# Optimization experiments

Hardware: AMD Instinct MI355X
Metric: run time of the kernel (lower is better)

The kernel has to match this reference:

```python
import jax, jax.numpy as jnp
import numpy as np

N = 100000
D = 128
E = 1600000
NUM_STEPS = 8
LAM0 = 1.0
LAM1 = 1.0
ALPHA = 1.0 / (1.0 + 0.0 + LAM0 + LAM1)  # args.alp == 0 path


def setup_inputs() -> dict:
    key = jax.random.key(0)
    ks = jax.random.split(key, 12)
    X = jax.random.normal(ks[0], (N, D), dtype=jnp.float32)
    # H init: normal(0, 1/in_features) + I  (notresidual=False branch)
    H1 = jax.random.normal(ks[1], (D, D), dtype=jnp.float32) * (1.0 / D) + jnp.eye(D, dtype=jnp.float32)
    H2 = jax.random.normal(ks[2], (D, D), dtype=jnp.float32) * (1.0 / D) + jnp.eye(D, dtype=jnp.float32)
    w_beta = jax.random.uniform(ks[3], (E,), dtype=jnp.float32)
    w_gamma = jax.random.uniform(ks[4], (E,), dtype=jnp.float32)
    d_beta = jax.random.uniform(ks[5], (N,), dtype=jnp.float32)
    d_gamma = jax.random.uniform(ks[6], (N,), dtype=jnp.float32)
    src_beta = jax.random.randint(ks[7], (E,), 0, N, dtype=jnp.int32)
    dst_beta = jax.random.randint(ks[8], (E,), 0, N, dtype=jnp.int32)
    src_gamma = jax.random.randint(ks[9], (E,), 0, N, dtype=jnp.int32)
    dst_gamma = jax.random.randint(ks[10], (E,), 0, N, dtype=jnp.int32)
    return {"X": X, "H1": H1, "H2": H2, "w_beta": w_beta, "w_gamma": w_gamma,
            "d_beta": d_beta, "d_gamma": d_gamma,
            "src_beta": src_beta, "dst_beta": dst_beta,
            "src_gamma": src_gamma, "dst_gamma": dst_gamma}


def _spmm(w, src, dst, Y):
    # (sparse A) @ Y with A[dst, src] = w
    return jax.ops.segment_sum(w[:, None] * Y[src], dst, num_segments=N)


def reference(X, H1, H2, w_beta, w_gamma, d_beta, d_gamma,
              src_beta, dst_beta, src_gamma, dst_gamma):
    # Q_tild = lam0*D_beta + lam1*D_gamma + I  (diagonal)
    q = LAM0 * d_beta + LAM1 * d_gamma + 1.0  # [N]
    S1 = H1 + H1.T
    P1 = H1 @ H1.T
    S2 = H2 + H2.T
    P2 = H2 @ H2.T
    Y0 = X
    Y = X
    for _ in range(NUM_STEPS):
        AbY = _spmm(w_beta, src_beta, dst_beta, Y)    # A_beta @ Y
        AgY = _spmm(w_gamma, src_gamma, dst_gamma, Y)  # A_gamma @ Y
        term_beta = AbY @ S1 - d_beta[:, None] * (Y @ P1)
        # L_gamma @ Y = D_gamma@Y - A_gamma@Y
        term_gamma = (d_gamma[:, None] * Y - AgY
                      + AgY @ S2 - d_gamma[:, None] * (Y @ P2))
        Y_hat = LAM0 * term_beta + Y0 + LAM1 * term_gamma
        Y = (1.0 - ALPHA) * Y + ALPHA * (Y_hat / q[:, None])
    return Y
```

## Files before the change

### kernel.cpp

```cpp
#include <hip/hip_runtime.h>
#include <cstdint>
#include <cstddef>

#define DD 128
#define ATS 68
#define WTS 130


__global__ void count2_k(const int* __restrict__ dstb, const int* __restrict__ dstg,
                         int* __restrict__ degb, int* __restrict__ degg, int E, int gE) {
    int b = blockIdx.x;
    const int* dst = (b < gE) ? dstb : dstg;
    int* deg = (b < gE) ? degb : degg;
    int i = ((b < gE) ? b : b - gE) * blockDim.x + threadIdx.x;
    if (i < E) atomicAdd(&deg[dst[i]], 1);
}

__global__ __launch_bounds__(1024) void scan2_k(const int* __restrict__ degb,
                                                const int* __restrict__ degg,
                                                int* __restrict__ rpb, int* __restrict__ rpg,
                                                int* __restrict__ curb, int* __restrict__ curg,
                                                int n) {
    const int* deg = (blockIdx.x == 0) ? degb : degg;
    int* rp = (blockIdx.x == 0) ? rpb : rpg;
    int* cur = (blockIdx.x == 0) ? curb : curg;
    __shared__ int sums[1024];
    int tid = threadIdx.x;
    int per = (n + 1023) >> 10;
    int start = tid * per;
    int end = min(start + per, n);
    int s = 0;
    for (int i = start; i < end; ++i) s += deg[i];
    sums[tid] = s;
    __syncthreads();
    for (int off = 1; off < 1024; off <<= 1) {
        int v = (tid >= off) ? sums[tid - off] : 0;
        __syncthreads();
        sums[tid] += v;
        __syncthreads();
    }
    int pre = (tid == 0) ? 0 : sums[tid - 1];
    for (int i = start; i < end; ++i) {
        rp[i] = pre;
        cur[i] = pre;
        pre += deg[i];
    }
    if (end == n) rp[n] = pre;
}

__global__ void fill2_k(const int* __restrict__ srcb, const int* __restrict__ dstb,
                        const float* __restrict__ wb,
                        const int* __restrict__ srcg, const int* __restrict__ dstg,
                        const float* __restrict__ wg,
                        int* __restrict__ curb, int* __restrict__ curg,
                        int2* __restrict__ eb, int2* __restrict__ eg, int E, int gE) {
    int b = blockIdx.x;
    bool isb = (b < gE);
    const int* src = isb ? srcb : srcg;
    const int* dst = isb ? dstb : dstg;
    const float* w = isb ? wb : wg;
    int* cur = isb ? curb : curg;
    int2* edges = isb ? eb : eg;
    int i = (isb ? b : b - gE) * blockDim.x + threadIdx.x;
    if (i < E) {
        int d = dst[i];
        int pos = atomicAdd(&cur[d], 1);
        edges[pos] = make_int2(src[i], __float_as_int(w[i]));
    }
}


__global__ __launch_bounds__(256) void prep_k(const float* __restrict__ H,
                                              float* __restrict__ P,
                                              float* __restrict__ S) {
    int idx = blockIdx.x * 256 + threadIdx.x;
    int i = idx >> 7, j = idx & 127;
    float acc = 0.f;
    for (int k = 0; k < DD; ++k) acc += H[i * DD + k] * H[j * DD + k];
    P[idx] = acc;
    S[idx] = H[i * DD + j] + H[j * DD + i];
}


__global__ __launch_bounds__(256, 8) void spmm2_k(
    const int* __restrict__ rpb, const int2* __restrict__ eb,
    const int* __restrict__ rpg, const int2* __restrict__ eg,
    const float* __restrict__ Y,
    float* __restrict__ outb, float* __restrict__ outg, int n)
{
    int node = blockIdx.x * 4 + (threadIdx.x >> 6);
    if (node >= n) return;
    int lane = threadIdx.x & 63;

    int jb = rpb[node], be = rpb[node + 1];
    int jg = rpg[node], ge = rpg[node + 1];
    float b0 = 0.f, b1 = 0.f, g0 = 0.f, g1 = 0.f;

    while (jb + 4 <= be && jg + 4 <= ge) {
        int2 x0 = eb[jb + 0], x1 = eb[jb + 1], x2 = eb[jb + 2], x3 = eb[jb + 3];
        int2 y0 = eg[jg + 0], y1 = eg[jg + 1], y2 = eg[jg + 2], y3 = eg[jg + 3];
        float2 fb0 = *((const float2*)(Y + (size_t)x0.x * DD) + lane);
        float2 fb1 = *((const float2*)(Y + (size_t)x1.x * DD) + lane);
        float2 fb2 = *((const float2*)(Y + (size_t)x2.x * DD) + lane);
        float2 fb3 = *((const float2*)(Y + (size_t)x3.x * DD) + lane);
        float2 fg0 = *((const float2*)(Y + (size_t)y0.x * DD) + lane);
        float2 fg1 = *((const float2*)(Y + (size_t)y1.x * DD) + lane);
        float2 fg2 = *((const float2*)(Y + (size_t)y2.x * DD) + lane);
        float2 fg3 = *((const float2*)(Y + (size_t)y3.x * DD) + lane);
        float wb0 = __int_as_float(x0.y), wb1 = __int_as_float(x1.y);
        float wb2 = __int_as_float(x2.y), wb3 = __int_as_float(x3.y);
        float wg0 = __int_as_float(y0.y), wg1 = __int_as_float(y1.y);
        float wg2 = __int_as_float(y2.y), wg3 = __int_as_float(y3.y);
        b0 += wb0 * fb0.x; b1 += wb0 * fb0.y;
        b0 += wb1 * fb1.x; b1 += wb1 * fb1.y;
        b0 += wb2 * fb2.x; b1 += wb2 * fb2.y;
        b0 += wb3 * fb3.x; b1 += wb3 * fb3.y;
        g0 += wg0 * fg0.x; g1 += wg0 * fg0.y;
        g0 += wg1 * fg1.x; g1 += wg1 * fg1.y;
        g0 += wg2 * fg2.x; g1 += wg2 * fg2.y;
        g0 += wg3 * fg3.x; g1 += wg3 * fg3.y;
        jb += 4; jg += 4;
    }
    while (jb + 4 <= be) {
        int2 x0 = eb[jb + 0], x1 = eb[jb + 1], x2 = eb[jb + 2], x3 = eb[jb + 3];
        float2 f0 = *((const float2*)(Y + (size_t)x0.x * DD) + lane);
        float2 f1 = *((const float2*)(Y + (size_t)x1.x * DD) + lane);
        float2 f2 = *((const float2*)(Y + (size_t)x2.x * DD) + lane);
        float2 f3 = *((const float2*)(Y + (size_t)x3.x * DD) + lane);
        float w0 = __int_as_float(x0.y), w1 = __int_as_float(x1.y);
        float w2 = __int_as_float(x2.y), w3 = __int_as_float(x3.y);
        b0 += w0 * f0.x; b1 += w0 * f0.y;
        b0 += w1 * f1.x; b1 += w1 * f1.y;
        b0 += w2 * f2.x; b1 += w2 * f2.y;
        b0 += w3 * f3.x; b1 += w3 * f3.y;
        jb += 4;
    }
    while (jg + 4 <= ge) {
        int2 y0 = eg[jg + 0], y1 = eg[jg + 1], y2 = eg[jg + 2], y3 = eg[jg + 3];
        float2 f0 = *((const float2*)(Y + (size_t)y0.x * DD) + lane);
        float2 f1 = *((const float2*)(Y + (size_t)y1.x * DD) + lane);
        float2 f2 = *((const float2*)(Y + (size_t)y2.x * DD) + lane);
        float2 f3 = *((const float2*)(Y + (size_t)y3.x * DD) + lane);
        float w0 = __int_as_float(y0.y), w1 = __int_as_float(y1.y);
        float w2 = __int_as_float(y2.y), w3 = __int_as_float(y3.y);
        g0 += w0 * f0.x; g1 += w0 * f0.y;
        g0 += w1 * f1.x; g1 += w1 * f1.y;
        g0 += w2 * f2.x; g1 += w2 * f2.y;
        g0 += w3 * f3.x; g1 += w3 * f3.y;
        jg += 4;
    }
    for (; jb < be; ++jb) {
        int2 e = eb[jb];
        float2 f = *((const float2*)(Y + (size_t)e.x * DD) + lane);
        float wv = __int_as_float(e.y);
        b0 += wv * f.x; b1 += wv * f.y;
    }
    for (; jg < ge; ++jg) {
        int2 e = eg[jg];
        float2 f = *((const float2*)(Y + (size_t)e.x * DD) + lane);
        float wv = __int_as_float(e.y);
        g0 += wv * f.x; g1 += wv * f.y;
    }
    *((float2*)(outb + (size_t)node * DD) + lane) = make_float2(b0, b1);
    *((float2*)(outg + (size_t)node * DD) + lane) = make_float2(g0, g1);
}


__global__ __launch_bounds__(1024, 8) void dense_vs_k(
    const float* __restrict__ Yc, const float* __restrict__ X,
    const float* __restrict__ AbY, const float* __restrict__ AgY,
    const float* __restrict__ db, const float* __restrict__ dg,
    const float* __restrict__ P1, const float* __restrict__ P2,
    const float* __restrict__ S1, const float* __restrict__ S2,
    float* __restrict__ Yn, int n)
{
    __shared__ float At[DD * ATS];

    const int tid  = threadIdx.x;
    const int lane = tid & 63;
    const int wid  = tid >> 6;
    const int cw   = wid << 3;
    const int c0   = __builtin_amdgcn_readfirstlane(cw);
    const int row0 = blockIdx.x * 64;
    const int rowc = min(row0 + lane, n - 1);

    auto stageT = [&](const float* __restrict__ G) {
        const float* gp = G + (size_t)rowc * DD + cw;
        float4 v0 = *reinterpret_cast<const float4*>(gp);
        float4 v1 = *reinterpret_cast<const float4*>(gp + 4);
        At[(cw + 0) * ATS + lane] = v0.x;
        At[(cw + 1) * ATS + lane] = v0.y;
        At[(cw + 2) * ATS + lane] = v0.z;
        At[(cw + 3) * ATS + lane] = v0.w;
        At[(cw + 4) * ATS + lane] = v1.x;
        At[(cw + 5) * ATS + lane] = v1.y;
        At[(cw + 6) * ATS + lane] = v1.z;
        At[(cw + 7) * ATS + lane] = v1.w;
    };

    const float dbv = db[rowc];
    const float dgv = dg[rowc];

    float acc[8];

    stageT(Yc);
    __syncthreads();

    {
        const float* xp = X + (size_t)rowc * DD + c0;
#pragma unroll
        for (int j = 0; j < 8; ++j)
            acc[j] = xp[j] + dgv * At[(c0 + j) * ATS + lane];
    }

    {
        const float* p1 = P1 + c0;
        const float* p2 = P2 + c0;
#pragma unroll 4
        for (int k = 0; k < DD; ++k) {
            float a = At[k * ATS + lane];
            float am1 = dbv * a;
            float am2 = dgv * a;
            const float* r1 = p1 + k * DD;
            const float* r2 = p2 + k * DD;
#pragma unroll
            for (int j = 0; j < 8; ++j)
                acc[j] -= am1 * r1[j] + am2 * r2[j];
        }
    }

    __syncthreads();
    stageT(AbY);
    __syncthreads();
    {
        const float* s1 = S1 + c0;
#pragma unroll 4
        for (int k = 0; k < DD; ++k) {
            float a = At[k * ATS + lane];
            const float* r = s1 + k * DD;
#pragma unroll
            for (int j = 0; j < 8; ++j)
                acc[j] += a * r[j];
        }
    }

    __syncthreads();
    stageT(AgY);
    __syncthreads();
    {
        const float* s2 = S2 + c0;
#pragma unroll 4
        for (int k = 0; k < DD; ++k) {
            float a = At[k * ATS + lane];
            const float* r = s2 + k * DD;
#pragma unroll
            for (int j = 0; j < 8; ++j)
                acc[j] += a * r[j];
        }
#pragma unroll
        for (int j = 0; j < 8; ++j)
            acc[j] -= At[(c0 + j) * ATS + lane];
    }

    {
        const float aq = (1.0f / 3.0f) / (dbv + dgv + 1.0f);
        const float* yp = Yc + (size_t)rowc * DD + c0;
#pragma unroll
        for (int j = 0; j < 8; ++j)
            acc[j] = (2.0f / 3.0f) * yp[j] + acc[j] * aq;
    }

    __syncthreads();
    {
        float* W = At;
#pragma unroll
        for (int j = 0; j < 8; ++j)
            W[lane * WTS + cw + j] = acc[j];
    }
    __syncthreads();
    {
        const float* W = At;
        int r2 = tid >> 4;
        int c2 = (tid & 15) << 3;
        int row2 = row0 + r2;
        if (row2 < n) {
            float ov[8];
#pragma unroll
            for (int j = 0; j < 8; ++j) ov[j] = W[r2 * WTS + c2 + j];
            float* op = Yn + (size_t)row2 * DD + c2;
            *reinterpret_cast<float4*>(op) = make_float4(ov[0], ov[1], ov[2], ov[3]);
            *reinterpret_cast<float4*>(op + 4) = make_float4(ov[4], ov[5], ov[6], ov[7]);
        }
    }
}


extern "C" void kernel_launch(void* const* d_in, const int* in_sizes, int n_in,
                              void* d_out, int out_size, void* d_ws, size_t ws_size,
                              hipStream_t stream) {
    const float* X   = (const float*)d_in[0];
    const float* H1  = (const float*)d_in[1];
    const float* H2  = (const float*)d_in[2];
    const float* wb  = (const float*)d_in[3];
    const float* wg  = (const float*)d_in[4];
    const float* db  = (const float*)d_in[5];
    const float* dg  = (const float*)d_in[6];
    const int* srcb  = (const int*)d_in[7];
    const int* dstb  = (const int*)d_in[8];
    const int* srcg  = (const int*)d_in[9];
    const int* dstg  = (const int*)d_in[10];
    const int N = in_sizes[5];
    const int E = in_sizes[3];
    float* Yout = (float*)d_out;

    char* p = (char*)d_ws;
    auto alloc = [&](size_t b) -> void* {
        void* r = (void*)p;
        p += (b + 255) & ~(size_t)255;
        return r;
    };
    float* P1 = (float*)alloc((size_t)DD * DD * 4);
    float* S1 = (float*)alloc((size_t)DD * DD * 4);
    float* P2 = (float*)alloc((size_t)DD * DD * 4);
    float* S2 = (float*)alloc((size_t)DD * DD * 4);
    int* degb = (int*)alloc((size_t)N * 4);
    int* degg = (int*)alloc((size_t)N * 4);
    int* rpb  = (int*)alloc((size_t)(N + 1) * 4);
    int* rpg  = (int*)alloc((size_t)(N + 1) * 4);
    int* curb = (int*)alloc((size_t)N * 4);
    int* curg = (int*)alloc((size_t)N * 4);
    int2* eb  = (int2*)alloc((size_t)E * 8);
    int2* eg  = (int2*)alloc((size_t)E * 8);
    float* AbY = (float*)alloc((size_t)N * DD * 4);
    float* AgY = (float*)alloc((size_t)N * DD * 4);
    float* Yw  = (float*)alloc((size_t)N * DD * 4);

    hipMemsetAsync(degb, 0, (size_t)N * 4, stream);
    hipMemsetAsync(degg, 0, (size_t)N * 4, stream);

    int gE = (E + 255) / 256;
    count2_k<<<2 * gE, 256, 0, stream>>>(dstb, dstg, degb, degg, E, gE);
    scan2_k<<<2, 1024, 0, stream>>>(degb, degg, rpb, rpg, curb, curg, N);
    fill2_k<<<2 * gE, 256, 0, stream>>>(srcb, dstb, wb, srcg, dstg, wg,
                                        curb, curg, eb, eg, E, gE);
    prep_k<<<64, 256, 0, stream>>>(H1, P1, S1);
    prep_k<<<64, 256, 0, stream>>>(H2, P2, S2);

    const float* Ycur = X;
    float* Ybufs[2] = {Yw, Yout};
    int gs = (N + 3) / 4;
    int gd = (N + 63) / 64;
    for (int s = 0; s < 8; ++s) {
        float* Yn = Ybufs[s & 1];
        spmm2_k<<<gs, 256, 0, stream>>>(rpb, eb, rpg, eg, Ycur, AbY, AgY, N);
        dense_vs_k<<<gd, 1024, 0, stream>>>(Ycur, X, AbY, AgY, db, dg,
                                            P1, P2, S1, S2, Yn, N);
        Ycur = Yn;
    }
}
```

Measured before the change: 4.438 ms.

## Apply dense projections before SpMM and fuse update into SpMM epilogue

Uses associativity to compute Y·S1, Y·(S2−I) and the residual term densely first, then gathers those projected rows in the SpMM and applies the final Y update in its epilogue. Removes the separate staging of AbY/AgY through the dense kernel and three sequential matmul passes. In exchange the dense kernel writes three full-size intermediates, and the two gathers now read distinct arrays, reducing cache reuse; the dense kernel also runs with lower occupancy bounds.

```diff
diff --git a/kernel.cpp b/kernel.cpp
--- a/kernel.cpp
+++ b/kernel.cpp
@@ -5,6 +5,8 @@
 #define DD 128
 #define ATS 68
 #define WTS 130
+
+typedef float f32x8 __attribute__((ext_vector_type(8)));
 
 
 __global__ void count2_k(const int* __restrict__ dstb, const int* __restrict__ dstg,
@@ -72,21 +74,147 @@
 
 __global__ __launch_bounds__(256) void prep_k(const float* __restrict__ H,
                                               float* __restrict__ P,
-                                              float* __restrict__ S) {
+                                              float* __restrict__ S, int sub_ident) {
     int idx = blockIdx.x * 256 + threadIdx.x;
     int i = idx >> 7, j = idx & 127;
     float acc = 0.f;
     for (int k = 0; k < DD; ++k) acc += H[i * DD + k] * H[j * DD + k];
     P[idx] = acc;
-    S[idx] = H[i * DD + j] + H[j * DD + i];
-}
-
-
-__global__ __launch_bounds__(256, 8) void spmm2_k(
+    float s = H[i * DD + j] + H[j * DD + i];
+    if (sub_ident && i == j) s -= 1.0f;
+    S[idx] = s;
+}
+
+
+__global__ void aq_k(const float* __restrict__ db, const float* __restrict__ dg,
+                     float* __restrict__ aq, int n) {
+    int i = blockIdx.x * blockDim.x + threadIdx.x;
+    if (i < n) aq[i] = (1.0f / 3.0f) / (db[i] + dg[i] + 1.0f);
+}
+
+
+__global__ __launch_bounds__(1024, 2) void denseY_k(
+    const float* __restrict__ Yc, const float* __restrict__ X,
+    const float* __restrict__ db, const float* __restrict__ dg,
+    const float* __restrict__ P1, const float* __restrict__ P2,
+    const float* __restrict__ S1, const float* __restrict__ S2m,
+    float* __restrict__ YS1, float* __restrict__ YSg, float* __restrict__ R, int n)
+{
+    __shared__ float At[DD * ATS];
+
+    const int tid  = threadIdx.x;
+    const int lane = tid & 63;
+    const int wid  = tid >> 6;
+    const int cw   = wid << 3;
+    const int c0   = __builtin_amdgcn_readfirstlane(cw);
+    const int row0 = blockIdx.x * 64;
+    const int rowc = min(row0 + lane, n - 1);
+
+    {
+        const float* gp = Yc + (size_t)rowc * DD + cw;
+        float4 v0 = *reinterpret_cast<const float4*>(gp);
+        float4 v1 = *reinterpret_cast<const float4*>(gp + 4);
+        At[(cw + 0) * ATS + lane] = v0.x;
+        At[(cw + 1) * ATS + lane] = v0.y;
+        At[(cw + 2) * ATS + lane] = v0.z;
+        At[(cw + 3) * ATS + lane] = v0.w;
+        At[(cw + 4) * ATS + lane] = v1.x;
+        At[(cw + 5) * ATS + lane] = v1.y;
+        At[(cw + 6) * ATS + lane] = v1.z;
+        At[(cw + 7) * ATS + lane] = v1.w;
+    }
+    __syncthreads();
+
+    const float dbv = db[rowc];
+    const float dgv = dg[rowc];
+
+    float a1[8], a2[8], aR[8];
+    {
+        const float* xp = X + (size_t)rowc * DD + cw;
+        float4 x0 = *reinterpret_cast<const float4*>(xp);
+        float4 x1 = *reinterpret_cast<const float4*>(xp + 4);
+        float xv[8] = {x0.x, x0.y, x0.z, x0.w, x1.x, x1.y, x1.z, x1.w};
+#pragma unroll
+        for (int j = 0; j < 8; ++j) {
+            a1[j] = 0.f; a2[j] = 0.f;
+            aR[j] = xv[j] + dgv * At[(c0 + j) * ATS + lane];
+        }
+    }
+
+    {
+        const f32x8* pS1 = reinterpret_cast<const f32x8*>(S1 + c0);
+        const f32x8* pS2 = reinterpret_cast<const f32x8*>(S2m + c0);
+        const f32x8* pP1 = reinterpret_cast<const f32x8*>(P1 + c0);
+        const f32x8* pP2 = reinterpret_cast<const f32x8*>(P2 + c0);
+#pragma unroll 2
+        for (int k = 0; k < DD; ++k) {
+            f32x8 b1 = pS1[k * 16];
+            f32x8 b2 = pS2[k * 16];
+            f32x8 b3 = pP1[k * 16];
+            f32x8 b4 = pP2[k * 16];
+            float a = At[k * ATS + lane];
+            float am1 = dbv * a;
+            float am2 = dgv * a;
+#pragma unroll
+            for (int j = 0; j < 8; ++j) {
+                a1[j] += a * b1[j];
+                a2[j] += a * b2[j];
+                aR[j] -= am1 * b3[j] + am2 * b4[j];
+            }
+        }
+    }
+
+    float* W = At;
+    const int r2 = tid >> 4;
+    const int c2 = (tid & 15) << 3;
+    const int row2 = row0 + r2;
+
+    __syncthreads();
+#pragma unroll
+    for (int j = 0; j < 8; ++j) W[lane * WTS + cw + j] = a1[j];
+    __syncthreads();
+    if (row2 < n) {
+        float ov[8];
+#pragma unroll
+        for (int j = 0; j < 8; ++j) ov[j] = W[r2 * WTS + c2 + j];
+        float* op = YS1 + (size_t)row2 * DD + c2;
+        *reinterpret_cast<float4*>(op) = make_float4(ov[0], ov[1], ov[2], ov[3]);
+        *reinterpret_cast<float4*>(op + 4) = make_float4(ov[4], ov[5], ov[6], ov[7]);
+    }
+    __syncthreads();
+#pragma unroll
+    for (int j = 0; j < 8; ++j) W[lane * WTS + cw + j] = a2[j];
+    __syncthreads();
+    if (row2 < n) {
+        float ov[8];
+#pragma unroll
+        for (int j = 0; j < 8; ++j) ov[j] = W[r2 * WTS + c2 + j];
+        float* op = YSg + (size_t)row2 * DD + c2;
+        *reinterpret_cast<float4*>(op) = make_float4(ov[0], ov[1], ov[2], ov[3]);
+        *reinterpret_cast<float4*>(op + 4) = make_float4(ov[4], ov[5], ov[6], ov[7]);
+    }
+    __syncthreads();
+#pragma unroll
+    for (int j = 0; j < 8; ++j) W[lane * WTS + cw + j] = aR[j];
+    __syncthreads();
+    if (row2 < n) {
+        float ov[8];
+#pragma unroll
+        for (int j = 0; j < 8; ++j) ov[j] = W[r2 * WTS + c2 + j];
+        float* op = R + (size_t)row2 * DD + c2;
+        *reinterpret_cast<float4*>(op) = make_float4(ov[0], ov[1], ov[2], ov[3]);
+        *reinterpret_cast<float4*>(op + 4) = make_float4(ov[4], ov[5], ov[6], ov[7]);
+    }
+}
+
+
+__global__ __launch_bounds__(256, 8) void spmmF_k(
     const int* __restrict__ rpb, const int2* __restrict__ eb,
     const int* __restrict__ rpg, const int2* __restrict__ eg,
-    const float* __restrict__ Y,
-    float* __restrict__ outb, float* __restrict__ outg, int n)
+    const float* __restrict__ YS1, const float* __restrict__ YSg,
+    const float* __restrict__ Yc, const float* __restrict__ R,
+    const float* __restrict__ aq,
+    float* __restrict__ Yn, int n)
 {
     int node = blockIdx.x * 4 + (threadIdx.x >> 6);
     if (node >= n) return;
@@ -99,14 +227,14 @@
     while (jb + 4 <= be && jg + 4 <= ge) {
         int2 x0 = eb[jb + 0], x1 = eb[jb + 1], x2 = eb[jb + 2], x3 = eb[jb + 3];
         int2 y0 = eg[jg + 0], y1 = eg[jg + 1], y2 = eg[jg + 2], y3 = eg[jg + 3];
-        float2 fb0 = *((const float2*)(Y + (size_t)x0.x * DD) + lane);
-        float2 fb1 = *((const float2*)(Y + (size_t)x1.x * DD) + lane);
-        float2 fb2 = *((const float2*)(Y + (size_t)x2.x * DD) + lane);
-        float2 fb3 = *((const float2*)(Y + (size_t)x3.x * DD) + lane);
-        float2 fg0 = *((const float2*)(Y + (size_t)y0.x * DD) + lane);
-        float2 fg1 = *((const float2*)(Y + (size_t)y1.x * DD) + lane);
-        float2 fg2 = *((const float2*)(Y + (size_t)y2.x * DD) + lane);
-        float2 fg3 = *((const float2*)(Y + (size_t)y3.x * DD) + lane);
+        float2 fb0 = *((const float2*)(YS1 + (size_t)x0.x * DD) + lane);
+        float2 fb1 = *((const float2*)(YS1 + (size_t)x1.x * DD) + lane);
+        float2 fb2 = *((const float2*)(YS1 + (size_t)x2.x * DD) + lane);
+        float2 fb3 = *((const float2*)(YS1 + (size_t)x3.x * DD) + lane);
+        float2 fg0 = *((const float2*)(YSg + (size_t)y0.x * DD) + lane);
+        float2 fg1 = *((const float2*)(YSg + (size_t)y1.x * DD) + lane);
+        float2 fg2 = *((const float2*)(YSg + (size_t)y2.x * DD) + lane);
+        float2 fg3 = *((const float2*)(YSg + (size_t)y3.x * DD) + lane);
         float wb0 = __int_as_float(x0.y), wb1 = __int_as_float(x1.y);
         float wb2 = __int_as_float(x2.y), wb3 = __int_as_float(x3.y);
         float wg0 = __int_as_float(y0.y), wg1 = __int_as_float(y1.y);
@@ -123,10 +251,10 @@
     }
     while (jb + 4 <= be) {
         int2 x0 = eb[jb + 0], x1 = eb[jb + 1], x2 = eb[jb + 2], x3 = eb[jb + 3];
-        float2 f0 = *((const float2*)(Y + (size_t)x0.x * DD) + lane);
-        float2 f1 = *((const float2*)(Y + (size_t)x1.x * DD) + lane);
-        float2 f2 = *((const float2*)(Y + (size_t)x2.x * DD) + lane);
-        float2 f3 = *((const float2*)(Y + (size_t)x3.x * DD) + lane);
+        float2 f0 = *((const float2*)(YS1 + (size_t)x0.x * DD) + lane);
+        float2 f1 = *((const float2*)(YS1 + (size_t)x1.x * DD) + lane);
+        float2 f2 = *((const float2*)(YS1 + (size_t)x2.x * DD) + lane);
+        float2 f3 = *((const float2*)(YS1 + (size_t)x3.x * DD) + lane);
         float w0 = __int_as_float(x0.y), w1 = __int_as_float(x1.y);
         float w2 = __int_as_float(x2.y), w3 = __int_as_float(x3.y);
         b0 += w0 * f0.x; b1 += w0 * f0.y;
@@ -137,10 +265,10 @@
     }
     while (jg + 4 <= ge) {
         int2 y0 = eg[jg + 0], y1 = eg[jg + 1], y2 = eg[jg + 2], y3 = eg[jg + 3];
-        float2 f0 = *((const float2*)(Y + (size_t)y0.x * DD) + lane);
-        float2 f1 = *((const float2*)(Y + (size_t)y1.x * DD) + lane);
-        float2 f2 = *((const float2*)(Y + (size_t)y2.x * DD) + lane);
-        float2 f3 = *((const float2*)(Y + (size_t)y3.x * DD) + lane);
+        float2 f0 = *((const float2*)(YSg + (size_t)y0.x * DD) + lane);
+        float2 f1 = *((const float2*)(YSg + (size_t)y1.x * DD) + lane);
+        float2 f2 = *((const float2*)(YSg + (size_t)y2.x * DD) + lane);
+        float2 f3 = *((const float2*)(YSg + (size_t)y3.x * DD) + lane);
         float w0 = __int_as_float(y0.y), w1 = __int_as_float(y1.y);
         float w2 = __int_as_float(y2.y), w3 = __int_as_float(y3.y);
         g0 += w0 * f0.x; g1 += w0 * f0.y;
@@ -151,147 +279,24 @@
     }
     for (; jb < be; ++jb) {
         int2 e = eb[jb];
-        float2 f = *((const float2*)(Y + (size_t)e.x * DD) + lane);
+        float2 f = *((const float2*)(YS1 + (size_t)e.x * DD) + lane);
         float wv = __int_as_float(e.y);
         b0 += wv * f.x; b1 += wv * f.y;
     }
     for (; jg < ge; ++jg) {
         int2 e = eg[jg];
-        float2 f = *((const float2*)(Y + (size_t)e.x * DD) + lane);
+        float2 f = *((const float2*)(YSg + (size_t)e.x * DD) + lane);
         float wv = __int_as_float(e.y);
         g0 += wv * f.x; g1 += wv * f.y;
     }
-    *((float2*)(outb + (size_t)node * DD) + lane) = make_float2(b0, b1);
-    *((float2*)(outg + (size_t)node * DD) + lane) = make_float2(g0, g1);
-}
-
-
-__global__ __launch_bounds__(1024, 8) void dense_vs_k(
-    const float* __restrict__ Yc, const float* __restrict__ X,
-    const float* __restrict__ AbY, const float* __restrict__ AgY,
-    const float* __restrict__ db, const float* __restrict__ dg,
-    const float* __restrict__ P1, const float* __restrict__ P2,
-    const float* __restrict__ S1, const float* __restrict__ S2,
-    float* __restrict__ Yn, int n)
-{
-    __shared__ float At[DD * ATS];
-
-    const int tid  = threadIdx.x;
-    const int lane = tid & 63;
-    const int wid  = tid >> 6;
-    const int cw   = wid << 3;
-    const int c0   = __builtin_amdgcn_readfirstlane(cw);
-    const int row0 = blockIdx.x * 64;
-    const int rowc = min(row0 + lane, n - 1);
-
-    auto stageT = [&](const float* __restrict__ G) {
-        const float* gp = G + (size_t)rowc * DD + cw;
-        float4 v0 = *reinterpret_cast<const float4*>(gp);
-        float4 v1 = *reinterpret_cast<const float4*>(gp + 4);
-        At[(cw + 0) * ATS + lane] = v0.x;
-        At[(cw + 1) * ATS + lane] = v0.y;
-        At[(cw + 2) * ATS + lane] = v0.z;
-        At[(cw + 3) * ATS + lane] = v0.w;
-        At[(cw + 4) * ATS + lane] = v1.x;
-        At[(cw + 5) * ATS + lane] = v1.y;
-        At[(cw + 6) * ATS + lane] = v1.z;
-        At[(cw + 7) * ATS + lane] = v1.w;
-    };
-
-    const float dbv = db[rowc];
-    const float dgv = dg[rowc];
-
-    float acc[8];
-
-    stageT(Yc);
-    __syncthreads();
-
-    {
-        const float* xp = X + (size_t)rowc * DD + c0;
-#pragma unroll
-        for (int j = 0; j < 8; ++j)
-            acc[j] = xp[j] + dgv * At[(c0 + j) * ATS + lane];
-    }
-
-    {
-        const float* p1 = P1 + c0;
-        const float* p2 = P2 + c0;
-#pragma unroll 4
-        for (int k = 0; k < DD; ++k) {
-            float a = At[k * ATS + lane];
-            float am1 = dbv * a;
-            float am2 = dgv * a;
-            const float* r1 = p1 + k * DD;
-            const float* r2 = p2 + k * DD;
-#pragma unroll
-            for (int j = 0; j < 8; ++j)
-                acc[j] -= am1 * r1[j] + am2 * r2[j];
-        }
-    }
-
-    __syncthreads();
-    stageT(AbY);
-    __syncthreads();
-    {
-        const float* s1 = S1 + c0;
-#pragma unroll 4
-        for (int k = 0; k < DD; ++k) {
-            float a = At[k * ATS + lane];
-            const float* r = s1 + k * DD;
-#pragma unroll
-            for (int j = 0; j < 8; ++j)
-                acc[j] += a * r[j];
-        }
-    }
-
-    __syncthreads();
-    stageT(AgY);
-    __syncthreads();
-    {
-        const float* s2 = S2 + c0;
-#pragma unroll 4
-        for (int k = 0; k < DD; ++k) {
-            float a = At[k * ATS + lane];
-            const float* r = s2 + k * DD;
-#pragma unroll
-            for (int j = 0; j < 8; ++j)
-                acc[j] += a * r[j];
-        }
-#pragma unroll
-        for (int j = 0; j < 8; ++j)
-            acc[j] -= At[(c0 + j) * ATS + lane];
-    }
-
-    {
-        const float aq = (1.0f / 3.0f) / (dbv + dgv + 1.0f);
-        const float* yp = Yc + (size_t)rowc * DD + c0;
-#pragma unroll
-        for (int j = 0; j < 8; ++j)
-            acc[j] = (2.0f / 3.0f) * yp[j] + acc[j] * aq;
-    }
-
-    __syncthreads();
-    {
-        float* W = At;
-#pragma unroll
-        for (int j = 0; j < 8; ++j)
-            W[lane * WTS + cw + j] = acc[j];
-    }
-    __syncthreads();
-    {
-        const float* W = At;
-        int r2 = tid >> 4;
-        int c2 = (tid & 15) << 3;
-        int row2 = row0 + r2;
-        if (row2 < n) {
-            float ov[8];
-#pragma unroll
-            for (int j = 0; j < 8; ++j) ov[j] = W[r2 * WTS + c2 + j];
-            float* op = Yn + (size_t)row2 * DD + c2;
-            *reinterpret_cast<float4*>(op) = make_float4(ov[0], ov[1], ov[2], ov[3]);
-            *reinterpret_cast<float4*>(op + 4) = make_float4(ov[4], ov[5], ov[6], ov[7]);
-        }
-    }
+
+    float2 y = *((const float2*)(Yc + (size_t)node * DD) + lane);
+    float2 r = *((const float2*)(R + (size_t)node * DD) + lane);
+    float aqv = aq[node];
+    float2 o;
+    o.x = (2.0f / 3.0f) * y.x + (b0 + g0 + r.x) * aqv;
+    o.y = (2.0f / 3.0f) * y.y + (b1 + g1 + r.y) * aqv;
+    *((float2*)(Yn + (size_t)node * DD) + lane) = o;
 }
 
 
@@ -319,20 +324,22 @@
         p += (b + 255) & ~(size_t)255;
         return r;
     };
-    float* P1 = (float*)alloc((size_t)DD * DD * 4);
-    float* S1 = (float*)alloc((size_t)DD * DD * 4);
-    float* P2 = (float*)alloc((size_t)DD * DD * 4);
-    float* S2 = (float*)alloc((size_t)DD * DD * 4);
+    float* P1  = (float*)alloc((size_t)DD * DD * 4);
+    float* S1  = (float*)alloc((size_t)DD * DD * 4);
+    float* P2  = (float*)alloc((size_t)DD * DD * 4);
+    float* S2m = (float*)alloc((size_t)DD * DD * 4);
     int* degb = (int*)alloc((size_t)N * 4);
     int* degg = (int*)alloc((size_t)N * 4);
     int* rpb  = (int*)alloc((size_t)(N + 1) * 4);
     int* rpg  = (int*)alloc((size_t)(N + 1) * 4);
     int* curb = (int*)alloc((size_t)N * 4);
     int* curg = (int*)alloc((size_t)N * 4);
+    float* aq = (float*)alloc((size_t)N * 4);
     int2* eb  = (int2*)alloc((size_t)E * 8);
     int2* eg  = (int2*)alloc((size_t)E * 8);
-    float* AbY = (float*)alloc((size_t)N * DD * 4);
-    float* AgY = (float*)alloc((size_t)N * DD * 4);
+    float* YS1 = (float*)alloc((size_t)N * DD * 4);
+    float* YSg = (float*)alloc((size_t)N * DD * 4);
+    float* R   = (float*)alloc((size_t)N * DD * 4);
     float* Yw  = (float*)alloc((size_t)N * DD * 4);
 
     hipMemsetAsync(degb, 0, (size_t)N * 4, stream);
@@ -343,8 +350,9 @@
     scan2_k<<<2, 1024, 0, stream>>>(degb, degg, rpb, rpg, curb, curg, N);
     fill2_k<<<2 * gE, 256, 0, stream>>>(srcb, dstb, wb, srcg, dstg, wg,
                                         curb, curg, eb, eg, E, gE);
-    prep_k<<<64, 256, 0, stream>>>(H1, P1, S1);
-    prep_k<<<64, 256, 0, stream>>>(H2, P2, S2);
+    prep_k<<<64, 256, 0, stream>>>(H1, P1, S1, 0);
+    prep_k<<<64, 256, 0, stream>>>(H2, P2, S2m, 1);
+    aq_k<<<(N + 255) / 256, 256, 0, stream>>>(db, dg, aq, N);
 
     const float* Ycur = X;
     float* Ybufs[2] = {Yw, Yout};
@@ -352,9 +360,10 @@
     int gd = (N + 63) / 64;
     for (int s = 0; s < 8; ++s) {
         float* Yn = Ybufs[s & 1];
-        spmm2_k<<<gs, 256, 0, stream>>>(rpb, eb, rpg, eg, Ycur, AbY, AgY, N);
-        dense_vs_k<<<gd, 1024, 0, stream>>>(Ycur, X, AbY, AgY, db, dg,
-                                            P1, P2, S1, S2, Yn, N);
+        denseY_k<<<gd, 1024, 0, stream>>>(Ycur, X, db, dg, P1, P2, S1, S2m,
+                                          YS1, YSg, R, N);
+        spmmF_k<<<gs, 256, 0, stream>>>(rpb, eb, rpg, eg, YS1, YSg,
+                                        Ycur, R, aq, Yn, N);
         Ycur = Yn;
     }
 }
```

Measured after the change: 4.200 ms. -5.4%, faster.
